# Optimization experiments

Measured on AMD Instinct MI355X. Metric: run time of the kernel, lower is better.

Reference implementation:

```python
import jax, jax.numpy as jnp
import numpy as np

OUT_FEATURES = 8192
IN_FEATURES = 8192
BATCH = 512


def setup_inputs() -> dict:
    key = jax.random.key(0)
    k_x, k_w, k_s = jax.random.split(key, 3)
    x = jax.random.normal(k_x, (BATCH, IN_FEATURES), dtype=jnp.float32)
    # packed int4 weights: each int holds two nibbles (values 0..255)
    packed_weight = jax.random.randint(k_w, (OUT_FEATURES, IN_FEATURES // 2), 0, 256, dtype=jnp.int32)
    # per-output-row scale (positive, as produced by abs-max quantization)
    scale = jax.random.uniform(k_s, (OUT_FEATURES, 1), dtype=jnp.float32) * 0.02 + 1e-4
    return {"x": x, "packed_weight": packed_weight, "scale": scale}


def reference(x, packed_weight, scale):
    # Unpack two 4-bit values per byte: high nibble first (matches torch loop:
    # col i <- packed >> 4 & 15, col i+1 <- packed & 15), then subtract zero-point 8.
    hi = (packed_weight >> 4) & 15
    lo = packed_weight & 15
    q = jnp.stack([hi, lo], axis=-1).reshape(OUT_FEATURES, IN_FEATURES) - 8  # [out, in] int
    w = q.astype(scale.dtype) * scale  # dequantized weight [out, in]
    # linear: y = x @ W^T
    return jnp.einsum('bi,oi->bo', x, w)
```

## Files before the change

### kernel.cpp

```cpp
#include <hip/hip_runtime.h>
#include <cstdint>
#include <cstddef>

#define IN_F 8192
#define OUT_F 8192
#define BATCH 512
#define KSPLIT 4
#define KSLICE (IN_F / KSPLIT)
#define BK 32
#define NIT (KSLICE / BK)
#define BM 128
#define BN 128

typedef __bf16 bf16x8 __attribute__((ext_vector_type(8)));
typedef float floatx4 __attribute__((ext_vector_type(4)));

__device__ __forceinline__ ushort f2bf(float f) {
  uint32_t u = __float_as_uint(f);
  u += 0x7FFFu + ((u >> 16) & 1u);
  return (ushort)(u >> 16);
}

__device__ __forceinline__ uint32_t dq(int p) {
  uint32_t u = (uint32_t)p;
  return (((u >> 4) & 0xFu) | ((u & 0xFu) << 16)) | 0x43004300u;
}

__device__ __forceinline__ void gl16(const void* g, uint32_t* l) {
  __builtin_amdgcn_global_load_lds(
      (const __attribute__((address_space(1))) uint32_t*)g,
      (__attribute__((address_space(3))) uint32_t*)l, 16, 0, 0);
}

__global__ __launch_bounds__(256) void cvt_rowsum(const float* __restrict__ x,
                                                  ushort* __restrict__ xb,
                                                  float* __restrict__ rowsum,
                                                  float* __restrict__ out) {
  const int b = blockIdx.x;
  const int t = threadIdx.x;
  const float4* xr = (const float4*)(x + (size_t)b * IN_F);
  ushort4* xo = (ushort4*)(xb + (size_t)b * IN_F);
  float4 z = {0.f, 0.f, 0.f, 0.f};
  float4* orow = (float4*)(out + (size_t)b * OUT_F);
  float s[4] = {0.f, 0.f, 0.f, 0.f};
#pragma unroll
  for (int i = 0; i < 8; ++i) {
    float4 v = xr[i * 256 + t];
    ushort4 o;
    o.x = f2bf(v.x); o.y = f2bf(v.y); o.z = f2bf(v.z); o.w = f2bf(v.w);
    xo[i * 256 + t] = o;
    orow[i * 256 + t] = z;
    s[i >> 1] += __uint_as_float((uint32_t)o.x << 16) + __uint_as_float((uint32_t)o.y << 16)
               + __uint_as_float((uint32_t)o.z << 16) + __uint_as_float((uint32_t)o.w << 16);
  }
  __shared__ float red[4][4];
  const int lane = t & 63, wid = t >> 6;
#pragma unroll
  for (int j = 0; j < 4; ++j) {
    float v = s[j];
#pragma unroll
    for (int off = 32; off >= 1; off >>= 1) v += __shfl_down(v, off, 64);
    if (lane == 0) red[wid][j] = v;
  }
  __syncthreads();
  if (t < 4) rowsum[t * BATCH + b] = red[0][t] + red[1][t] + red[2][t] + red[3][t];
}

__global__ __launch_bounds__(256, 2) void qgemm(const ushort* __restrict__ xb,
                                                const int* __restrict__ pw,
                                                const float* __restrict__ scale,
                                                const float* __restrict__ rowsum,
                                                float* __restrict__ out) {
  __shared__ uint32_t As[2 * BM * 16];
  __shared__ uint32_t Bs[2 * BN * 16];

  const int tid = threadIdx.x;
  const int lane = tid & 63;
  const int w = tid >> 6;
  const int wm = w & 1, wn = w >> 1;
  const int lr = lane & 15, lq = lane >> 4;

  const int n0 = blockIdx.x * BN;
  const int m0 = blockIdx.y * BM;
  const int ks = blockIdx.z;

  const int qsw = (lane & 3) ^ ((lane >> 3) & 3);
  const char* aG = (const char*)xb
      + (size_t)(m0 + w * 32 + (lane >> 2)) * (IN_F * 2)
      + (size_t)ks * (KSLICE * 2) + qsw * 16;
  uint32_t* aL = As + (w * 32) * 16;

  const int br = tid >> 1, bh = tid & 1;
  const char* bG = (const char*)pw + (size_t)(n0 + br) * (IN_F * 2)
      + (size_t)ks * (KSLICE * 2) + bh * 32;
  uint32_t* bW = Bs + br * 16;
  const int bkey = (tid >> 2) & 3;
  const int c0 = bh * 2, c1 = bh * 2 + 1;

  const int rkey = (lr >> 1) & 3;
  const uint32_t* aR = As + (wm * 64 + lr) * 16 + (lq ^ rkey) * 4;
  const uint32_t* bR = Bs + (wn * 64 + lr) * 16 + (lq ^ rkey) * 4;

  floatx4 acc[4][4] = {};

  gl16(aG, aL);
  gl16(aG + (size_t)16 * (IN_F * 2), aL + 256);
  int4 pb0 = *(const int4*)bG;
  int4 pb1 = *(const int4*)(bG + 16);

  for (int it = 0; it < NIT; ++it) {
    const int off = (it & 1) * (BM * 16);
    int4 u0, u1;
    u0.x = dq(pb0.x); u0.y = dq(pb0.y); u0.z = dq(pb0.z); u0.w = dq(pb0.w);
    u1.x = dq(pb1.x); u1.y = dq(pb1.y); u1.z = dq(pb1.z); u1.w = dq(pb1.w);
    *(int4*)(bW + off + ((c0 ^ bkey) << 2)) = u0;
    *(int4*)(bW + off + ((c1 ^ bkey) << 2)) = u1;
    __syncthreads();
    if (it + 1 < NIT) {
      const int off2 = ((it + 1) & 1) * (BM * 16);
      const char* aN = aG + (size_t)(it + 1) * 64;
      gl16(aN, aL + off2);
      gl16(aN + (size_t)16 * (IN_F * 2), aL + off2 + 256);
      const char* bN = bG + (size_t)(it + 1) * 64;
      pb0 = *(const int4*)bN;
      pb1 = *(const int4*)(bN + 16);
    }
    bf16x8 av[4], bv[4];
#pragma unroll
    for (int i = 0; i < 4; ++i) av[i] = *(const bf16x8*)(aR + off + i * 256);
#pragma unroll
    for (int i = 0; i < 4; ++i) bv[i] = *(const bf16x8*)(bR + off + i * 256);
#pragma unroll
    for (int mi = 0; mi < 4; ++mi)
#pragma unroll
      for (int ni = 0; ni < 4; ++ni)
        acc[mi][ni] = __builtin_amdgcn_mfma_f32_16x16x32_bf16(av[mi], bv[ni],
                                                              acc[mi][ni], 0, 0, 0);
  }

  const int om = m0 + wm * 64 + lq * 4;
  const int on = n0 + wn * 64 + lr;
  float scv[4];
#pragma unroll
  for (int ni = 0; ni < 4; ++ni) scv[ni] = scale[on + ni * 16];
  float rsv[4][4];
#pragma unroll
  for (int mi = 0; mi < 4; ++mi)
#pragma unroll
    for (int rr = 0; rr < 4; ++rr)
      rsv[mi][rr] = rowsum[ks * BATCH + om + mi * 16 + rr];

#pragma unroll
  for (int mi = 0; mi < 4; ++mi)
#pragma unroll
    for (int ni = 0; ni < 4; ++ni) {
      const float s = scv[ni];
      float* op = out + (size_t)(om + mi * 16) * OUT_F + (on + ni * 16);
#pragma unroll
      for (int rr = 0; rr < 4; ++rr)
        atomicAdd(op + (size_t)rr * OUT_F, s * (acc[mi][ni][rr] - 136.f * rsv[mi][rr]));
    }
}

extern "C" void kernel_launch(void* const* d_in, const int* in_sizes, int n_in,
                              void* d_out, int out_size, void* d_ws, size_t ws_size,
                              hipStream_t stream) {
  const float* x = (const float*)d_in[0];
  const int* pw = (const int*)d_in[1];
  const float* scale = (const float*)d_in[2];
  float* out = (float*)d_out;

  ushort* xb = (ushort*)d_ws;
  float* rowsum = (float*)((char*)d_ws + (size_t)BATCH * IN_F * sizeof(ushort));

  cvt_rowsum<<<BATCH, 256, 0, stream>>>(x, xb, rowsum, out);
  dim3 grid(OUT_F / BN, BATCH / BM, KSPLIT);
  qgemm<<<grid, 256, 0, stream>>>(xb, pw, scale, rowsum, out);
}
```

Before: 308.4 us.

## Enlarge qgemm to 256x256x64 tiles with 8 waves and interleaved dequant stores

Moves the quantized GEMM from 128x128 tiles with BK=32 and 4 waves to 256x256 tiles with BK=64 and 8 waves. Each wave now computes a 128x64 sub-tile, which raises operand reuse per LDS read. The B dequant stores for the next tile are interleaved between MFMA blocks, with s_setprio around the MFMAs and hand-placed waitcnt/barrier instructions. The aim is less global and LDS traffic per FLOP and better overlap of loads with compute. In exchange the grid shrinks to 32x2x4 = 256 blocks, each block uses 128KB of LDS, and register pressure rises with 32 accumulator tiles, so occupancy and load balance may suffer.

```diff
diff --git a/kernel.cpp b/kernel.cpp
--- a/kernel.cpp
+++ b/kernel.cpp
@@ -7,10 +7,10 @@
 #define BATCH 512
 #define KSPLIT 4
 #define KSLICE (IN_F / KSPLIT)
-#define BK 32
-#define NIT (KSLICE / BK)
-#define BM 128
-#define BN 128
+#define BK 64
+#define TILES (KSLICE / BK)
+#define BM 256
+#define BN 256
 
 typedef __bf16 bf16x8 __attribute__((ext_vector_type(8)));
 typedef float floatx4 __attribute__((ext_vector_type(4)));
@@ -66,100 +66,141 @@
   if (t < 4) rowsum[t * BATCH + b] = red[0][t] + red[1][t] + red[2][t] + red[3][t];
 }
 
-__global__ __launch_bounds__(256, 2) void qgemm(const ushort* __restrict__ xb,
+__global__ __launch_bounds__(512, 2) void qgemm(const ushort* __restrict__ xb,
                                                 const int* __restrict__ pw,
                                                 const float* __restrict__ scale,
                                                 const float* __restrict__ rowsum,
                                                 float* __restrict__ out) {
-  __shared__ uint32_t As[2 * BM * 16];
-  __shared__ uint32_t Bs[2 * BN * 16];
+  __shared__ uint32_t As[2 * BM * 32];
+  __shared__ uint32_t Bs[2 * BN * 32];
 
   const int tid = threadIdx.x;
   const int lane = tid & 63;
   const int w = tid >> 6;
-  const int wm = w & 1, wn = w >> 1;
+  const int wm = w >> 2, wn = w & 3;
   const int lr = lane & 15, lq = lane >> 4;
 
   const int n0 = blockIdx.x * BN;
   const int m0 = blockIdx.y * BM;
   const int ks = blockIdx.z;
 
-  const int qsw = (lane & 3) ^ ((lane >> 3) & 3);
-  const char* aG = (const char*)xb
-      + (size_t)(m0 + w * 32 + (lane >> 2)) * (IN_F * 2)
-      + (size_t)ks * (KSLICE * 2) + qsw * 16;
-  uint32_t* aL = As + (w * 32) * 16;
-
-  const int br = tid >> 1, bh = tid & 1;
-  const char* bG = (const char*)pw + (size_t)(n0 + br) * (IN_F * 2)
-      + (size_t)ks * (KSLICE * 2) + bh * 32;
-  uint32_t* bW = Bs + br * 16;
-  const int bkey = (tid >> 2) & 3;
-  const int c0 = bh * 2, c1 = bh * 2 + 1;
-
-  const int rkey = (lr >> 1) & 3;
-  const uint32_t* aR = As + (wm * 64 + lr) * 16 + (lq ^ rkey) * 4;
-  const uint32_t* bR = Bs + (wn * 64 + lr) * 16 + (lq ^ rkey) * 4;
-
-  floatx4 acc[4][4] = {};
-
-  gl16(aG, aL);
-  gl16(aG + (size_t)16 * (IN_F * 2), aL + 256);
-  int4 pb0 = *(const int4*)bG;
-  int4 pb1 = *(const int4*)(bG + 16);
-
-  for (int it = 0; it < NIT; ++it) {
-    const int off = (it & 1) * (BM * 16);
-    int4 u0, u1;
-    u0.x = dq(pb0.x); u0.y = dq(pb0.y); u0.z = dq(pb0.z); u0.w = dq(pb0.w);
-    u1.x = dq(pb1.x); u1.y = dq(pb1.y); u1.z = dq(pb1.z); u1.w = dq(pb1.w);
-    *(int4*)(bW + off + ((c0 ^ bkey) << 2)) = u0;
-    *(int4*)(bW + off + ((c1 ^ bkey) << 2)) = u1;
-    __syncthreads();
-    if (it + 1 < NIT) {
-      const int off2 = ((it + 1) & 1) * (BM * 16);
-      const char* aN = aG + (size_t)(it + 1) * 64;
-      gl16(aN, aL + off2);
-      gl16(aN + (size_t)16 * (IN_F * 2), aL + off2 + 256);
-      const char* bN = bG + (size_t)(it + 1) * 64;
-      pb0 = *(const int4*)bN;
-      pb1 = *(const int4*)(bN + 16);
-    }
+  const char* aSrc = (const char*)xb
+      + (size_t)(m0 + w * 32 + (lane >> 3)) * (IN_F * 2)
+      + (size_t)ks * (KSLICE * 2)
+      + (size_t)((((lane & 7) ^ ((lane >> 3) & 7)) * 16));
+  uint32_t* aDst = As + (w * 32) * 32;
+
+  const int rt = tid >> 1;
+  const int c0 = (tid & 1) * 2;
+  const int rk = rt & 7;
+  const int* bSrc = pw + (size_t)(n0 + rt) * (IN_F / 2) + ks * (KSLICE / 2);
+
+  const int key = lr & 7;
+  const int aOff = (wm * 128 + lr) * 32 + ((lq ^ key) * 4);
+  const int bOff = (wn * 64 + lr) * 32 + ((lq ^ key) * 4);
+
+  floatx4 acc[8][4] = {};
+
+  auto stB = [&](int nb, int q, int4 p) {
+    int4 u;
+    u.x = dq(p.x); u.y = dq(p.y); u.z = dq(p.z); u.w = dq(p.w);
+    *(int4*)(Bs + nb * 8192 + rt * 32 + ((q ^ rk) * 4)) = u;
+  };
+
+#define RD_BV(kh)                                                            \
+  _Pragma("unroll") for (int fn = 0; fn < 4; ++fn)                           \
+      bv[fn] = *(const bf16x8*)(Bs + (((bOff + fn * 512) ^ ((kh)*16)) + buf * 8192));
+#define RD_AV(mh, kh)                                                        \
+  _Pragma("unroll") for (int fm = 0; fm < 4; ++fm)                           \
+      av[fm] = *(const bf16x8*)(As + (((aOff + (mh)*2048 + fm * 512) ^ ((kh)*16)) + buf * 8192));
+#define MFMA_BLK(mh)                                                         \
+  __builtin_amdgcn_s_setprio(1);                                             \
+  _Pragma("unroll") for (int fm = 0; fm < 4; ++fm)                           \
+      _Pragma("unroll") for (int fn = 0; fn < 4; ++fn)                       \
+          acc[(mh)*4 + fm][fn] = __builtin_amdgcn_mfma_f32_16x16x32_bf16(    \
+              av[fm], bv[fn], acc[(mh)*4 + fm][fn], 0, 0, 0);                \
+  __builtin_amdgcn_s_setprio(0);
+
+  {
+    int4 p0 = *(const int4*)(bSrc + c0 * 4);
+    int4 p1 = *(const int4*)(bSrc + c0 * 4 + 4);
+    int4 p2 = *(const int4*)(bSrc + (c0 + 4) * 4);
+    int4 p3 = *(const int4*)(bSrc + (c0 + 4) * 4 + 4);
+    stB(0, c0, p0); stB(0, c0 + 1, p1); stB(0, c0 + 4, p2); stB(0, c0 + 5, p3);
+    gl16(aSrc, aDst);
+    gl16(aSrc + 131072, aDst + 256);
+    gl16(aSrc + 262144, aDst + 512);
+    gl16(aSrc + 393216, aDst + 768);
+    asm volatile("s_waitcnt lgkmcnt(0)" ::: "memory");
+  }
+
+  for (int t = 0; t < TILES - 1; ++t) {
+    const int buf = t & 1, nb = buf ^ 1;
+    const int* bs = bSrc + (t + 1) * 32;
+    int4 pb0 = *(const int4*)(bs + c0 * 4);
+    int4 pb1 = *(const int4*)(bs + c0 * 4 + 4);
+    int4 pb2 = *(const int4*)(bs + (c0 + 4) * 4);
+    int4 pb3 = *(const int4*)(bs + (c0 + 4) * 4 + 4);
+    const char* as = aSrc + (size_t)(t + 1) * 128;
+    gl16(as, aDst + nb * 8192);
+    gl16(as + 131072, aDst + nb * 8192 + 256);
+    gl16(as + 262144, aDst + nb * 8192 + 512);
+    gl16(as + 393216, aDst + nb * 8192 + 768);
+    asm volatile("s_waitcnt vmcnt(8)" ::: "memory");
+    asm volatile("s_barrier" ::: "memory");
+
     bf16x8 av[4], bv[4];
-#pragma unroll
-    for (int i = 0; i < 4; ++i) av[i] = *(const bf16x8*)(aR + off + i * 256);
-#pragma unroll
-    for (int i = 0; i < 4; ++i) bv[i] = *(const bf16x8*)(bR + off + i * 256);
-#pragma unroll
-    for (int mi = 0; mi < 4; ++mi)
-#pragma unroll
-      for (int ni = 0; ni < 4; ++ni)
-        acc[mi][ni] = __builtin_amdgcn_mfma_f32_16x16x32_bf16(av[mi], bv[ni],
-                                                              acc[mi][ni], 0, 0, 0);
-  }
-
-  const int om = m0 + wm * 64 + lq * 4;
+    RD_BV(0);
+    RD_AV(0, 0); MFMA_BLK(0);
+    stB(nb, c0, pb0); stB(nb, c0 + 1, pb1);
+    RD_AV(1, 0); MFMA_BLK(1);
+    RD_BV(1);
+    RD_AV(0, 1); MFMA_BLK(0);
+    stB(nb, c0 + 4, pb2); stB(nb, c0 + 5, pb3);
+    RD_AV(1, 1); MFMA_BLK(1);
+
+    asm volatile("s_waitcnt lgkmcnt(0)" ::: "memory");
+    asm volatile("s_barrier" ::: "memory");
+  }
+
+  {
+    const int buf = (TILES - 1) & 1;
+    asm volatile("s_waitcnt vmcnt(0)" ::: "memory");
+    asm volatile("s_barrier" ::: "memory");
+    bf16x8 av[4], bv[4];
+    RD_BV(0);
+    RD_AV(0, 0); MFMA_BLK(0);
+    RD_AV(1, 0); MFMA_BLK(1);
+    RD_BV(1);
+    RD_AV(0, 1); MFMA_BLK(0);
+    RD_AV(1, 1); MFMA_BLK(1);
+  }
+
+  const int omb = m0 + wm * 128 + lq * 4;
   const int on = n0 + wn * 64 + lr;
   float scv[4];
 #pragma unroll
-  for (int ni = 0; ni < 4; ++ni) scv[ni] = scale[on + ni * 16];
-  float rsv[4][4];
-#pragma unroll
-  for (int mi = 0; mi < 4; ++mi)
+  for (int fn = 0; fn < 4; ++fn) scv[fn] = scale[on + fn * 16];
+  float rsv[8][4];
+#pragma unroll
+  for (int fmg = 0; fmg < 8; ++fmg)
 #pragma unroll
     for (int rr = 0; rr < 4; ++rr)
-      rsv[mi][rr] = rowsum[ks * BATCH + om + mi * 16 + rr];
-
-#pragma unroll
-  for (int mi = 0; mi < 4; ++mi)
-#pragma unroll
-    for (int ni = 0; ni < 4; ++ni) {
-      const float s = scv[ni];
-      float* op = out + (size_t)(om + mi * 16) * OUT_F + (on + ni * 16);
+      rsv[fmg][rr] = rowsum[ks * BATCH + omb + fmg * 16 + rr];
+
+#pragma unroll
+  for (int fmg = 0; fmg < 8; ++fmg)
+#pragma unroll
+    for (int fn = 0; fn < 4; ++fn) {
+      const float s = scv[fn];
+      float* op = out + (size_t)(omb + fmg * 16) * OUT_F + (on + fn * 16);
 #pragma unroll
       for (int rr = 0; rr < 4; ++rr)
-        atomicAdd(op + (size_t)rr * OUT_F, s * (acc[mi][ni][rr] - 136.f * rsv[mi][rr]));
+        atomicAdd(op + (size_t)rr * OUT_F, s * (acc[fmg][fn][rr] - 136.f * rsv[fmg][rr]));
     }
+#undef RD_BV
+#undef RD_AV
+#undef MFMA_BLK
 }
 
 extern "C" void kernel_launch(void* const* d_in, const int* in_sizes, int n_in,
@@ -175,5 +216,5 @@
 
   cvt_rowsum<<<BATCH, 256, 0, stream>>>(x, xb, rowsum, out);
   dim3 grid(OUT_F / BN, BATCH / BM, KSPLIT);
-  qgemm<<<grid, 256, 0, stream>>>(xb, pw, scale, rowsum, out);
-}
+  qgemm<<<grid, 512, 0, stream>>>(xb, pw, scale, rowsum, out);
+}
```

After: 302.4 us. No clear change (-1.9%).
